# Performance work log

Hardware: AMD Instinct MI355X
Metric: run time of the kernel (lower is better)

Reference implementation:

```python
import jax, jax.numpy as jnp
import numpy as np

N_HEAD, D_K, D_V = 8, 64, 64
TOPK = 16
B, N_R, N_W = 256, 64, 64
D_READ = D_WRITE = D_OUT = 512
TEMP = float(np.power(D_K, 0.5))
EPS = 1e-7  # 10e-8 in original Sparse_attention


def sparse_attention(a, top_k):
    # a: (rows, n); RIMs Sparse_attention: threshold at k-th largest, clamp, renormalize
    if a.shape[-1] <= top_k:
        return a
    delta = jax.lax.top_k(a, top_k)[0][..., -1:] + EPS
    w = jnp.clip(a - delta, 0.0, None)
    return w / (jnp.sum(w, axis=-1, keepdims=True) + EPS)


def setup_inputs() -> dict:
    key = jax.random.key(0)
    ks = jax.random.split(key, 8)
    q = jax.random.normal(ks[0], (B, N_R, D_READ), dtype=jnp.float32)
    k = jax.random.normal(ks[1], (B, N_W, D_WRITE), dtype=jnp.float32)
    v = jax.random.normal(ks[2], (B, N_W, D_WRITE), dtype=jnp.float32)
    # GroupLinearLayer weights: (num_blocks, d_in, n_head*d)
    Wq = 0.02 * jax.random.normal(ks[3], (N_R, D_READ, N_HEAD * D_K), dtype=jnp.float32)
    Wk = 0.02 * jax.random.normal(ks[4], (N_W, D_WRITE, N_HEAD * D_K), dtype=jnp.float32)
    Wv = 0.02 * jax.random.normal(ks[5], (N_W, D_WRITE, N_HEAD * D_V), dtype=jnp.float32)
    fc_w = 0.02 * jax.random.normal(ks[6], (D_OUT, N_HEAD * D_V), dtype=jnp.float32)
    fc_b = jnp.zeros((D_OUT,), dtype=jnp.float32)
    gate_w = 0.02 * jax.random.normal(ks[7], (D_OUT, N_HEAD * D_V), dtype=jnp.float32)
    gate_b = jnp.zeros((D_OUT,), dtype=jnp.float32)
    return {"q": q, "k": k, "v": v, "Wq": Wq, "Wk": Wk, "Wv": Wv,
            "fc_w": fc_w, "fc_b": fc_b, "gate_w": gate_w, "gate_b": gate_b}


def reference(q, k, v, Wq, Wk, Wv, fc_w, fc_b, gate_w, gate_b):
    # grouped per-block projections: out[b,n] = x[b,n] @ W[n]
    qp = jnp.einsum('bnd,nde->bne', q, Wq).reshape(B, N_R, N_HEAD, D_K)
    kp = jnp.einsum('bnd,nde->bne', k, Wk).reshape(B, N_W, N_HEAD, D_K)
    vp = jnp.einsum('bnd,nde->bne', v, Wv).reshape(B, N_W, N_HEAD, D_V)
    # (H*B, len, d) with head-major leading dim, matching permute(2,0,1,3).view(-1,...)
    qh = qp.transpose(2, 0, 1, 3).reshape(N_HEAD * B, N_R, D_K)
    kh = kp.transpose(2, 0, 1, 3).reshape(N_HEAD * B, N_W, D_K)
    vh = vp.transpose(2, 0, 1, 3).reshape(N_HEAD * B, N_W, D_V)
    scores = jnp.einsum('ijk,ilk->ijl', qh, kh) / TEMP          # (HB, Nr, Nw)
    a = jnp.exp(jnp.max(scores, axis=-1, keepdims=True))        # (HB, Nr, 1)
    # flag=True: softmax over the query-block dim (permute/softmax/reshape)
    a = jax.nn.softmax(a[..., 0], axis=-1)                      # (HB, Nr)
    a = sparse_attention(a, TOPK)                               # (HB, Nr)
    attn = a[..., None]                                         # (HB, Nr, 1)
    # einsum 'ijk,ikl->ijl' with attn's k-dim == 1 broadcasts: attn * sum_k v
    out = attn * jnp.sum(vh, axis=1, keepdims=True)             # (HB, Nr, Dv)
    out = out.reshape(N_HEAD, B, N_R, D_V).transpose(1, 2, 0, 3).reshape(B, N_R, N_HEAD * D_V)
    fc_out = out @ fc_w.T + fc_b
    gate = jax.nn.sigmoid(out @ gate_w.T + gate_b)
    output = gate * jnp.tanh(fc_out)                            # residual=True gating
    return output
```

## Files before the change

### kernel.cpp

```cpp
#include <hip/hip_runtime.h>
#include <stdint.h>

#define B_    256
#define NR    64
#define NW    64
#define DIN   512
#define NH    8
#define DK    64
#define E_    512
#define TEMP_INV 0.125f
#define EPSV  1e-7f

typedef unsigned short u16;
typedef unsigned int   u32;
typedef __attribute__((ext_vector_type(4))) float  floatx4;
typedef __attribute__((ext_vector_type(8))) short  shortx8;
typedef __attribute__((ext_vector_type(4))) short  shortx4;
typedef __attribute__((ext_vector_type(2))) u32    uintx2;

__device__ __forceinline__ u32 asu(float f) { union { float f; u32 u; } c; c.f = f; return c.u; }
__device__ __forceinline__ float asf(u32 u) { union { u32 u; float f; } c; c.u = u; return c.f; }

__device__ __forceinline__ u32 packhi(u32 x, u32 y) {
    return (x >> 16) | (y & 0xFFFF0000u);
}

#define PST 40

__global__ __launch_bounds__(256)
void proj_kernel(const float* __restrict__ q, const float* __restrict__ kk_,
                 const float* __restrict__ v,
                 const float* __restrict__ Wq, const float* __restrict__ Wk,
                 const float* __restrict__ Wv,
                 float* __restrict__ qp, float* __restrict__ kp,
                 float* __restrict__ vsum)
{
    const float* X; const float* W; float* dst = nullptr; bool vmode = false;
    if (blockIdx.z == 0)      { X = q;   W = Wq; dst = qp; }
    else if (blockIdx.z == 1) { X = kk_; W = Wk; dst = kp; }
    else                      { X = v;   W = Wv; vmode = true; }

    const int n  = blockIdx.y;
    const int m0 = (blockIdx.x >> 2) * 128;
    const int n0 = (blockIdx.x & 3) * 128;

    __shared__ u16 Ah[128 * PST];
    __shared__ u16 Al[128 * PST];
    __shared__ u16 Bh[128 * PST];
    __shared__ u16 Bl[128 * PST];

    const int tid  = threadIdx.x;
    const int lane = tid & 63;
    const int wave = tid >> 6;
    const int wm   = (wave >> 1) * 64;
    const int wn   = (wave & 1) * 64;
    const int l15  = lane & 15;
    const int quad = lane >> 4;

    floatx4 acc[4][4];
#pragma unroll
    for (int i = 0; i < 4; i++)
#pragma unroll
        for (int j = 0; j < 4; j++) acc[i][j] = (floatx4){0.f, 0.f, 0.f, 0.f};

    const int arow  = tid >> 1;
    const int ahalf = tid & 1;
    const float* aptr = X + ((size_t)(m0 + arow) * NW + n) * DIN + ahalf * 16;
    const int ec0  = (tid & 31) * 4;
    const int kgrp = tid >> 5;
    const float* wbase = W + (size_t)n * (DIN * E_) + n0 + ec0;

    floatx4 pa[4], pb[4];
#pragma unroll
    for (int c = 0; c < 4; c++) pa[c] = *(const floatx4*)(aptr + c * 4);
#pragma unroll
    for (int j = 0; j < 4; j++) pb[j] = *(const floatx4*)(wbase + (size_t)(kgrp * 4 + j) * E_);

    for (int it = 0; it < 16; it++) {
        const int k0 = it * 32;

#pragma unroll
        for (int c = 0; c < 4; c++) {
            u32 x = asu(pa[c].x), y = asu(pa[c].y), z = asu(pa[c].z), w = asu(pa[c].w);
            u32 h01 = packhi(x, y), h23 = packhi(z, w);
            float r0 = pa[c].x - asf(x & 0xFFFF0000u);
            float r1 = pa[c].y - asf(y & 0xFFFF0000u);
            float r2 = pa[c].z - asf(z & 0xFFFF0000u);
            float r3 = pa[c].w - asf(w & 0xFFFF0000u);
            u32 l01 = packhi(asu(r0), asu(r1)), l23 = packhi(asu(r2), asu(r3));
            *(uintx2*)&Ah[arow * PST + ahalf * 16 + c * 4] = (uintx2){h01, h23};
            if (!vmode)
                *(uintx2*)&Al[arow * PST + ahalf * 16 + c * 4] = (uintx2){l01, l23};
        }
#pragma unroll
        for (int e = 0; e < 4; e++) {
            u32 x0 = asu(pb[0][e]), x1 = asu(pb[1][e]), x2 = asu(pb[2][e]), x3 = asu(pb[3][e]);
            u32 h01 = packhi(x0, x1), h23 = packhi(x2, x3);
            *(uintx2*)&Bh[(ec0 + e) * PST + kgrp * 4] = (uintx2){h01, h23};
            if (!vmode) {
                float r0 = pb[0][e] - asf(x0 & 0xFFFF0000u);
                float r1 = pb[1][e] - asf(x1 & 0xFFFF0000u);
                float r2 = pb[2][e] - asf(x2 & 0xFFFF0000u);
                float r3 = pb[3][e] - asf(x3 & 0xFFFF0000u);
                u32 l01 = packhi(asu(r0), asu(r1)), l23 = packhi(asu(r2), asu(r3));
                *(uintx2*)&Bl[(ec0 + e) * PST + kgrp * 4] = (uintx2){l01, l23};
            }
        }

        if (it < 15) {
            const int kn = k0 + 32;
#pragma unroll
            for (int c = 0; c < 4; c++) pa[c] = *(const floatx4*)(aptr + kn + c * 4);
#pragma unroll
            for (int j = 0; j < 4; j++)
                pb[j] = *(const floatx4*)(wbase + (size_t)(kn + kgrp * 4 + j) * E_);
        }

        __syncthreads();

        shortx8 afh[4], afl[4], bfh[4], bfl[4];
#pragma unroll
        for (int mi = 0; mi < 4; mi++) {
            afh[mi] = *(const shortx8*)&Ah[(wm + mi * 16 + l15) * PST + quad * 8];
            if (!vmode)
                afl[mi] = *(const shortx8*)&Al[(wm + mi * 16 + l15) * PST + quad * 8];
        }
#pragma unroll
        for (int ni = 0; ni < 4; ni++) {
            bfh[ni] = *(const shortx8*)&Bh[(wn + ni * 16 + l15) * PST + quad * 8];
            if (!vmode)
                bfl[ni] = *(const shortx8*)&Bl[(wn + ni * 16 + l15) * PST + quad * 8];
        }
#pragma unroll
        for (int mi = 0; mi < 4; mi++)
#pragma unroll
            for (int ni = 0; ni < 4; ni++) {
                acc[mi][ni] = __builtin_amdgcn_mfma_f32_16x16x32_bf16(
                    afh[mi], bfh[ni], acc[mi][ni], 0, 0, 0);
                if (!vmode) {
                    acc[mi][ni] = __builtin_amdgcn_mfma_f32_16x16x32_bf16(
                        afh[mi], bfl[ni], acc[mi][ni], 0, 0, 0);
                    acc[mi][ni] = __builtin_amdgcn_mfma_f32_16x16x32_bf16(
                        afl[mi], bfh[ni], acc[mi][ni], 0, 0, 0);
                }
            }
        __syncthreads();
    }

    if (!vmode) {
#pragma unroll
        for (int mi = 0; mi < 4; mi++) {
            int rowb = m0 + wm + mi * 16 + quad * 4;
#pragma unroll
            for (int ni = 0; ni < 4; ni++) {
                int col = n0 + wn + ni * 16 + l15;
#pragma unroll
                for (int r = 0; r < 4; r++)
                    dst[((size_t)(rowb + r) * NW + n) * E_ + col] = acc[mi][ni][r];
            }
        }
    } else {
#pragma unroll
        for (int mi = 0; mi < 4; mi++) {
            int rowb = m0 + wm + mi * 16 + quad * 4;
#pragma unroll
            for (int ni = 0; ni < 4; ni++) {
                int col = n0 + wn + ni * 16 + l15;
#pragma unroll
                for (int r = 0; r < 4; r++)
                    atomicAdd(&vsum[(size_t)(rowb + r) * E_ + col], acc[mi][ni][r]);
            }
        }
    }
}

__global__ __launch_bounds__(256)
void attn_kernel(const float* __restrict__ qp, const float* __restrict__ kp,
                 float* __restrict__ attnT)
{
    const int h = blockIdx.x >> 8;
    const int b = blockIdx.x & 255;

    __shared__ float qs[64 * 68];
    __shared__ float ks[64 * 68];
    __shared__ float mred[4][64];

    const int t    = threadIdx.x;
    const int w    = t >> 6;
    const int lane = t & 63;

#pragma unroll
    for (int s = 0; s < 4; s++) {
        int f = s * 256 + t;
        int row = f >> 4, c4 = (f & 15) * 4;
        *(floatx4*)&qs[row * 68 + c4] =
            *(const floatx4*)&qp[((size_t)(b * NR + row)) * E_ + h * DK + c4];
        *(floatx4*)&ks[row * 68 + c4] =
            *(const floatx4*)&kp[((size_t)(b * NW + row)) * E_ + h * DK + c4];
    }
    __syncthreads();

    floatx4 qr[16];
#pragma unroll
    for (int c = 0; c < 16; c++) qr[c] = *(const floatx4*)&qs[lane * 68 + c * 4];

    float mloc = -1e30f;
#pragma unroll 4
    for (int ll = 0; ll < 16; ll++) {
        int l = w * 16 + ll;
        floatx4 a4 = (floatx4){0.f, 0.f, 0.f, 0.f};
#pragma unroll
        for (int c = 0; c < 16; c++) {
            floatx4 kv = *(const floatx4*)&ks[l * 68 + c * 4];
            a4.x = fmaf(qr[c].x, kv.x, a4.x);
            a4.y = fmaf(qr[c].y, kv.y, a4.y);
            a4.z = fmaf(qr[c].z, kv.z, a4.z);
            a4.w = fmaf(qr[c].w, kv.w, a4.w);
        }
        float s = (a4.x + a4.y) + (a4.z + a4.w);
        mloc = fmaxf(mloc, s);
    }
    mred[w][lane] = mloc;
    __syncthreads();

    if (t < 64) {
        float m = fmaxf(fmaxf(mred[0][lane], mred[1][lane]),
                        fmaxf(mred[2][lane], mred[3][lane])) * TEMP_INV;
        float e = expf(m);
        float mx = e;
#pragma unroll
        for (int d = 1; d < 64; d <<= 1) mx = fmaxf(mx, __shfl_xor(mx, d));
        float tt = expf(e - mx);
        float S = tt;
#pragma unroll
        for (int d = 1; d < 64; d <<= 1) S += __shfl_xor(S, d);
        float s = tt / S;

        float cur = s, v16 = 0.f;
        for (int itk = 0; itk < 16; itk++) {
            float mv = cur;
#pragma unroll
            for (int d = 1; d < 64; d <<= 1) mv = fmaxf(mv, __shfl_xor(mv, d));
            unsigned long long bal = __ballot(cur == mv);
            int first = __ffsll(bal) - 1;
            if (lane == first) cur = -1e30f;
            v16 = mv;
        }
        float delta = v16 + EPSV;
        float ww = fmaxf(s - delta, 0.f);
        float sw = ww;
#pragma unroll
        for (int d = 1; d < 64; d <<= 1) sw += __shfl_xor(sw, d);
        attnT[((size_t)b * NR + lane) * NH + h] = ww / (sw + EPSV);
    }
}

__global__ __launch_bounds__(256)
void fcv_kernel(const float* __restrict__ vsum, const float* __restrict__ fc_w,
                const float* __restrict__ gate_w, float* __restrict__ fcv,
                float* __restrict__ gatev)
{
    const int ohalf = blockIdx.x >> 2;
    const int bq    = blockIdx.x & 3;
    const int h     = blockIdx.y;
    const float* W  = blockIdx.z ? gate_w : fc_w;
    float* out      = blockIdx.z ? gatev : fcv;
    const int o     = ohalf * 256 + threadIdx.x;

    __shared__ float vs[64 * 64];
#pragma unroll
    for (int i = 0; i < 16; i++) {
        int idx = i * 256 + threadIdx.x;
        int bb = idx >> 6, d = idx & 63;
        vs[idx] = vsum[(size_t)(bq * 64 + bb) * E_ + h * DK + d];
    }
    floatx4 wr[16];
#pragma unroll
    for (int c = 0; c < 16; c++)
        wr[c] = *(const floatx4*)(W + (size_t)o * E_ + h * DK + c * 4);
    __syncthreads();

    for (int bb = 0; bb < 64; bb++) {
        const floatx4* vr = (const floatx4*)&vs[bb * 64];
        float a = 0.f;
#pragma unroll
        for (int c = 0; c < 16; c++) {
            floatx4 vv = vr[c];
            a += vv.x * wr[c].x + vv.y * wr[c].y + vv.z * wr[c].z + vv.w * wr[c].w;
        }
        out[((size_t)(bq * 64 + bb) * NH + h) * E_ + o] = a;
    }
}

__global__ __launch_bounds__(256)
void final_kernel(const float* __restrict__ fcv, const float* __restrict__ gatev,
                  const float* __restrict__ attnT, const float* __restrict__ fc_b,
                  const float* __restrict__ gate_b, float* __restrict__ out)
{
    const int b = blockIdx.x;
    const int tid = threadIdx.x;
    __shared__ float ats[NR * NH];

    ats[tid]       = attnT[(size_t)b * NR * NH + tid];
    ats[256 + tid] = attnT[(size_t)b * NR * NH + 256 + tid];

    float fr[2][8], gr[2][8];
#pragma unroll
    for (int half = 0; half < 2; half++) {
        int o = half * 256 + tid;
#pragma unroll
        for (int hh = 0; hh < 8; hh++) {
            fr[half][hh] = fcv[((size_t)b * NH + hh) * E_ + o];
            gr[half][hh] = gatev[((size_t)b * NH + hh) * E_ + o];
        }
    }
    float bfc0 = fc_b[tid],   bfc1 = fc_b[256 + tid];
    float bgt0 = gate_b[tid], bgt1 = gate_b[256 + tid];
    __syncthreads();

    for (int r = 0; r < NR; r++) {
        float a[8];
#pragma unroll
        for (int hh = 0; hh < 8; hh++) a[hh] = ats[r * NH + hh];
#pragma unroll
        for (int half = 0; half < 2; half++) {
            int o = half * 256 + tid;
            float fc = half ? bfc1 : bfc0;
            float gt = half ? bgt1 : bgt0;
#pragma unroll
            for (int hh = 0; hh < 8; hh++) {
                fc = fmaf(a[hh], fr[half][hh], fc);
                gt = fmaf(a[hh], gr[half][hh], gt);
            }
            float g = 1.f / (1.f + __expf(-gt));
            out[((size_t)(b * NR + r)) * E_ + o] = g * tanhf(fc);
        }
    }
}

extern "C" void kernel_launch(void* const* d_in, const int* in_sizes, int n_in,
                              void* d_out, int out_size, void* d_ws, size_t ws_size,
                              hipStream_t stream)
{
    const float* q      = (const float*)d_in[0];
    const float* k      = (const float*)d_in[1];
    const float* v      = (const float*)d_in[2];
    const float* Wq     = (const float*)d_in[3];
    const float* Wk     = (const float*)d_in[4];
    const float* Wv     = (const float*)d_in[5];
    const float* fc_w   = (const float*)d_in[6];
    const float* fc_b   = (const float*)d_in[7];
    const float* gate_w = (const float*)d_in[8];
    const float* gate_b = (const float*)d_in[9];
    float* out = (float*)d_out;

    char* ws = (char*)d_ws;
    float* qp    = (float*)(ws);
    float* kp    = (float*)(ws + 33554432);
    float* vsum  = (float*)(ws + 67108864);
    float* attnT = (float*)(ws + 67108864 + 524288);
    float* fcv   = (float*)(ws + 67108864 + 2 * 524288);
    float* gatev = (float*)(ws + 67108864 + 2 * 524288 + 4194304);

    hipMemsetAsync(vsum, 0, 524288, stream);

    hipLaunchKernelGGL(proj_kernel, dim3(8, 64, 3), dim3(256), 0, stream,
                       q, k, v, Wq, Wk, Wv, qp, kp, vsum);
    hipLaunchKernelGGL(attn_kernel, dim3(2048), dim3(256), 0, stream, qp, kp, attnT);
    hipLaunchKernelGGL(fcv_kernel, dim3(8, 8, 2), dim3(256), 0, stream,
                       vsum, fc_w, gate_w, fcv, gatev);
    hipLaunchKernelGGL(final_kernel, dim3(256), dim3(256), 0, stream,
                       fcv, gatev, attnT, fc_b, gate_b, out);
}
```

Measured before the change: 426.2 us.

## Store q/k projections in fp16, use fdot2 attention, relayout shared tiles

The projection kernel now writes the q and k projections as fp16 instead of fp32, halving that intermediate traffic. The attention kernel reads q into registers and computes scores with packed fp16 dot products straight from global k, dropping the shared-memory staging. The projection's shared-memory tiles are relaid out in a k-chunk-major format, and its block-index mapping is reordered to group work on the same weight block. The fcv kernel gets twice as many blocks and tanh is replaced by an exp-based formula. The fp16 scores reduce precision, which risks changing the max and top-k selection.

```diff
diff --git a/kernel.cpp b/kernel.cpp
--- a/kernel.cpp
+++ b/kernel.cpp
@@ -13,41 +13,51 @@
 
 typedef unsigned short u16;
 typedef unsigned int   u32;
-typedef __attribute__((ext_vector_type(4))) float  floatx4;
-typedef __attribute__((ext_vector_type(8))) short  shortx8;
-typedef __attribute__((ext_vector_type(4))) short  shortx4;
-typedef __attribute__((ext_vector_type(2))) u32    uintx2;
+typedef _Float16 f16;
+typedef __attribute__((ext_vector_type(2))) float    floatx2;
+typedef __attribute__((ext_vector_type(4))) float    floatx4;
+typedef __attribute__((ext_vector_type(8))) short    shortx8;
+typedef __attribute__((ext_vector_type(4))) u32      uintx4;
+typedef __attribute__((ext_vector_type(2))) _Float16 halfx2;
 
 __device__ __forceinline__ u32 asu(float f) { union { float f; u32 u; } c; c.f = f; return c.u; }
 __device__ __forceinline__ float asf(u32 u) { union { u32 u; float f; } c; c.u = u; return c.f; }
-
-__device__ __forceinline__ u32 packhi(u32 x, u32 y) {
-    return (x >> 16) | (y & 0xFFFF0000u);
-}
-
-#define PST 40
+__device__ __forceinline__ u32 packhi(float x, float y) {
+    return (asu(x) >> 16) | (asu(y) & 0xFFFF0000u);
+}
+__device__ __forceinline__ float hi_of(float x) { return asf(asu(x) & 0xFFFF0000u); }
+__device__ __forceinline__ halfx2 h2(u32 u) { union { u32 u; halfx2 h; } c; c.u = u; return c.h; }
+
+#if __has_builtin(__builtin_amdgcn_fdot2)
+#define FDOT2(a, b, c) __builtin_amdgcn_fdot2((a), (b), (c), false)
+#else
+__device__ __forceinline__ float FDOT2(halfx2 a, halfx2 b, float c) {
+    return fmaf((float)a.y, (float)b.y, fmaf((float)a.x, (float)b.x, c));
+}
+#endif
 
 __global__ __launch_bounds__(256)
 void proj_kernel(const float* __restrict__ q, const float* __restrict__ kk_,
                  const float* __restrict__ v,
                  const float* __restrict__ Wq, const float* __restrict__ Wk,
                  const float* __restrict__ Wv,
-                 float* __restrict__ qp, float* __restrict__ kp,
+                 f16* __restrict__ qp, f16* __restrict__ kp,
                  float* __restrict__ vsum)
 {
-    const float* X; const float* W; float* dst = nullptr; bool vmode = false;
+    const float* X; const float* W; f16* dst = nullptr; bool vmode = false;
     if (blockIdx.z == 0)      { X = q;   W = Wq; dst = qp; }
     else if (blockIdx.z == 1) { X = kk_; W = Wk; dst = kp; }
     else                      { X = v;   W = Wv; vmode = true; }
 
-    const int n  = blockIdx.y;
-    const int m0 = (blockIdx.x >> 2) * 128;
-    const int n0 = (blockIdx.x & 3) * 128;
-
-    __shared__ u16 Ah[128 * PST];
-    __shared__ u16 Al[128 * PST];
-    __shared__ u16 Bh[128 * PST];
-    __shared__ u16 Bl[128 * PST];
+    const int n  = blockIdx.x * 8 + (blockIdx.y & 7);
+    const int t  = blockIdx.y >> 3;
+    const int m0 = (t >> 2) * 128;
+    const int n0 = (t & 3) * 128;
+
+    __shared__ u16 Ah[4096];
+    __shared__ u16 Al[4096];
+    __shared__ u16 Bh[4096];
+    __shared__ u16 Bl[4096];
 
     const int tid  = threadIdx.x;
     const int lane = tid & 63;
@@ -66,54 +76,57 @@
     const int arow  = tid >> 1;
     const int ahalf = tid & 1;
     const float* aptr = X + ((size_t)(m0 + arow) * NW + n) * DIN + ahalf * 16;
-    const int ec0  = (tid & 31) * 4;
-    const int kgrp = tid >> 5;
-    const float* wbase = W + (size_t)n * (DIN * E_) + n0 + ec0;
-
-    floatx4 pa[4], pb[4];
+    const int kq = tid >> 6;
+    const int p  = tid & 63;
+    const float* wptr = W + (size_t)n * (DIN * E_) + n0 + 2 * p;
+
+    floatx4 pa[4]; floatx2 pb[8];
 #pragma unroll
     for (int c = 0; c < 4; c++) pa[c] = *(const floatx4*)(aptr + c * 4);
 #pragma unroll
-    for (int j = 0; j < 4; j++) pb[j] = *(const floatx4*)(wbase + (size_t)(kgrp * 4 + j) * E_);
+    for (int j = 0; j < 8; j++) pb[j] = *(const floatx2*)(wptr + (size_t)(kq * 8 + j) * E_);
 
     for (int it = 0; it < 16; it++) {
-        const int k0 = it * 32;
-
-#pragma unroll
-        for (int c = 0; c < 4; c++) {
-            u32 x = asu(pa[c].x), y = asu(pa[c].y), z = asu(pa[c].z), w = asu(pa[c].w);
-            u32 h01 = packhi(x, y), h23 = packhi(z, w);
-            float r0 = pa[c].x - asf(x & 0xFFFF0000u);
-            float r1 = pa[c].y - asf(y & 0xFFFF0000u);
-            float r2 = pa[c].z - asf(z & 0xFFFF0000u);
-            float r3 = pa[c].w - asf(w & 0xFFFF0000u);
-            u32 l01 = packhi(asu(r0), asu(r1)), l23 = packhi(asu(r2), asu(r3));
-            *(uintx2*)&Ah[arow * PST + ahalf * 16 + c * 4] = (uintx2){h01, h23};
-            if (!vmode)
-                *(uintx2*)&Al[arow * PST + ahalf * 16 + c * 4] = (uintx2){l01, l23};
-        }
-#pragma unroll
-        for (int e = 0; e < 4; e++) {
-            u32 x0 = asu(pb[0][e]), x1 = asu(pb[1][e]), x2 = asu(pb[2][e]), x3 = asu(pb[3][e]);
-            u32 h01 = packhi(x0, x1), h23 = packhi(x2, x3);
-            *(uintx2*)&Bh[(ec0 + e) * PST + kgrp * 4] = (uintx2){h01, h23};
+        {
+            u32 h[8], l[8];
+#pragma unroll
+            for (int c = 0; c < 4; c++) {
+                h[2 * c]     = packhi(pa[c].x, pa[c].y);
+                h[2 * c + 1] = packhi(pa[c].z, pa[c].w);
+                float r0 = pa[c].x - hi_of(pa[c].x), r1 = pa[c].y - hi_of(pa[c].y);
+                float r2 = pa[c].z - hi_of(pa[c].z), r3 = pa[c].w - hi_of(pa[c].w);
+                l[2 * c]     = packhi(r0, r1);
+                l[2 * c + 1] = packhi(r2, r3);
+            }
+            *(uintx4*)&Ah[(2 * ahalf + 0) * 1024 + arow * 8] = (uintx4){h[0], h[1], h[2], h[3]};
+            *(uintx4*)&Ah[(2 * ahalf + 1) * 1024 + arow * 8] = (uintx4){h[4], h[5], h[6], h[7]};
             if (!vmode) {
-                float r0 = pb[0][e] - asf(x0 & 0xFFFF0000u);
-                float r1 = pb[1][e] - asf(x1 & 0xFFFF0000u);
-                float r2 = pb[2][e] - asf(x2 & 0xFFFF0000u);
-                float r3 = pb[3][e] - asf(x3 & 0xFFFF0000u);
-                u32 l01 = packhi(asu(r0), asu(r1)), l23 = packhi(asu(r2), asu(r3));
-                *(uintx2*)&Bl[(ec0 + e) * PST + kgrp * 4] = (uintx2){l01, l23};
+                *(uintx4*)&Al[(2 * ahalf + 0) * 1024 + arow * 8] = (uintx4){l[0], l[1], l[2], l[3]};
+                *(uintx4*)&Al[(2 * ahalf + 1) * 1024 + arow * 8] = (uintx4){l[4], l[5], l[6], l[7]};
+            }
+        }
+#pragma unroll
+        for (int eo = 0; eo < 2; eo++) {
+            float x0 = pb[0][eo], x1 = pb[1][eo], x2 = pb[2][eo], x3 = pb[3][eo];
+            float x4 = pb[4][eo], x5 = pb[5][eo], x6 = pb[6][eo], x7 = pb[7][eo];
+            uintx4 hv = (uintx4){packhi(x0, x1), packhi(x2, x3), packhi(x4, x5), packhi(x6, x7)};
+            *(uintx4*)&Bh[kq * 1024 + eo * 512 + p * 8] = hv;
+            if (!vmode) {
+                uintx4 lv = (uintx4){packhi(x0 - hi_of(x0), x1 - hi_of(x1)),
+                                     packhi(x2 - hi_of(x2), x3 - hi_of(x3)),
+                                     packhi(x4 - hi_of(x4), x5 - hi_of(x5)),
+                                     packhi(x6 - hi_of(x6), x7 - hi_of(x7))};
+                *(uintx4*)&Bl[kq * 1024 + eo * 512 + p * 8] = lv;
             }
         }
 
         if (it < 15) {
-            const int kn = k0 + 32;
+            const int kn = it * 32 + 32;
 #pragma unroll
             for (int c = 0; c < 4; c++) pa[c] = *(const floatx4*)(aptr + kn + c * 4);
 #pragma unroll
-            for (int j = 0; j < 4; j++)
-                pb[j] = *(const floatx4*)(wbase + (size_t)(kn + kgrp * 4 + j) * E_);
+            for (int j = 0; j < 8; j++)
+                pb[j] = *(const floatx2*)(wptr + (size_t)(kn + kq * 8 + j) * E_);
         }
 
         __syncthreads();
@@ -121,15 +134,16 @@
         shortx8 afh[4], afl[4], bfh[4], bfl[4];
 #pragma unroll
         for (int mi = 0; mi < 4; mi++) {
-            afh[mi] = *(const shortx8*)&Ah[(wm + mi * 16 + l15) * PST + quad * 8];
-            if (!vmode)
-                afl[mi] = *(const shortx8*)&Al[(wm + mi * 16 + l15) * PST + quad * 8];
+            int R = wm + mi * 16 + l15;
+            afh[mi] = *(const shortx8*)&Ah[quad * 1024 + R * 8];
+            if (!vmode) afl[mi] = *(const shortx8*)&Al[quad * 1024 + R * 8];
         }
 #pragma unroll
         for (int ni = 0; ni < 4; ni++) {
-            bfh[ni] = *(const shortx8*)&Bh[(wn + ni * 16 + l15) * PST + quad * 8];
-            if (!vmode)
-                bfl[ni] = *(const shortx8*)&Bl[(wn + ni * 16 + l15) * PST + quad * 8];
+            int e = wn + ni * 16 + l15;
+            int off = quad * 1024 + (e & 1) * 512 + (e >> 1) * 8;
+            bfh[ni] = *(const shortx8*)&Bh[off];
+            if (!vmode) bfl[ni] = *(const shortx8*)&Bl[off];
         }
 #pragma unroll
         for (int mi = 0; mi < 4; mi++)
@@ -156,7 +170,7 @@
                 int col = n0 + wn + ni * 16 + l15;
 #pragma unroll
                 for (int r = 0; r < 4; r++)
-                    dst[((size_t)(rowb + r) * NW + n) * E_ + col] = acc[mi][ni][r];
+                    dst[((size_t)(rowb + r) * NW + n) * E_ + col] = (f16)acc[mi][ni][r];
             }
         }
     } else {
@@ -175,58 +189,45 @@
 }
 
 __global__ __launch_bounds__(256)
-void attn_kernel(const float* __restrict__ qp, const float* __restrict__ kp,
+void attn_kernel(const f16* __restrict__ qp, const f16* __restrict__ kp,
                  float* __restrict__ attnT)
 {
     const int h = blockIdx.x >> 8;
     const int b = blockIdx.x & 255;
-
-    __shared__ float qs[64 * 68];
-    __shared__ float ks[64 * 68];
     __shared__ float mred[4][64];
 
     const int t    = threadIdx.x;
     const int w    = t >> 6;
     const int lane = t & 63;
 
-#pragma unroll
-    for (int s = 0; s < 4; s++) {
-        int f = s * 256 + t;
-        int row = f >> 4, c4 = (f & 15) * 4;
-        *(floatx4*)&qs[row * 68 + c4] =
-            *(const floatx4*)&qp[((size_t)(b * NR + row)) * E_ + h * DK + c4];
-        *(floatx4*)&ks[row * 68 + c4] =
-            *(const floatx4*)&kp[((size_t)(b * NW + row)) * E_ + h * DK + c4];
-    }
+    const f16* qrow = qp + ((size_t)(b * NR + lane)) * E_ + h * DK;
+    halfx2 qreg[32];
+#pragma unroll
+    for (int c = 0; c < 8; c++) {
+        uintx4 u = *(const uintx4*)(qrow + c * 8);
+        qreg[c * 4 + 0] = h2(u.x); qreg[c * 4 + 1] = h2(u.y);
+        qreg[c * 4 + 2] = h2(u.z); qreg[c * 4 + 3] = h2(u.w);
+    }
+
+    float m = -1e30f;
+    for (int ll = 0; ll < 16; ll++) {
+        int lu = __builtin_amdgcn_readfirstlane(w * 16 + ll);
+        const u32* k32 = (const u32*)(kp + ((size_t)(b * NW + lu)) * E_ + h * DK);
+        float a0 = 0.f, a1 = 0.f;
+#pragma unroll
+        for (int c = 0; c < 32; c += 2) {
+            a0 = FDOT2(qreg[c],     h2(k32[c]),     a0);
+            a1 = FDOT2(qreg[c + 1], h2(k32[c + 1]), a1);
+        }
+        m = fmaxf(m, a0 + a1);
+    }
+    mred[w][lane] = m;
     __syncthreads();
 
-    floatx4 qr[16];
-#pragma unroll
-    for (int c = 0; c < 16; c++) qr[c] = *(const floatx4*)&qs[lane * 68 + c * 4];
-
-    float mloc = -1e30f;
-#pragma unroll 4
-    for (int ll = 0; ll < 16; ll++) {
-        int l = w * 16 + ll;
-        floatx4 a4 = (floatx4){0.f, 0.f, 0.f, 0.f};
-#pragma unroll
-        for (int c = 0; c < 16; c++) {
-            floatx4 kv = *(const floatx4*)&ks[l * 68 + c * 4];
-            a4.x = fmaf(qr[c].x, kv.x, a4.x);
-            a4.y = fmaf(qr[c].y, kv.y, a4.y);
-            a4.z = fmaf(qr[c].z, kv.z, a4.z);
-            a4.w = fmaf(qr[c].w, kv.w, a4.w);
-        }
-        float s = (a4.x + a4.y) + (a4.z + a4.w);
-        mloc = fmaxf(mloc, s);
-    }
-    mred[w][lane] = mloc;
-    __syncthreads();
-
     if (t < 64) {
-        float m = fmaxf(fmaxf(mred[0][lane], mred[1][lane]),
-                        fmaxf(mred[2][lane], mred[3][lane])) * TEMP_INV;
-        float e = expf(m);
+        float mm = fmaxf(fmaxf(mred[0][lane], mred[1][lane]),
+                         fmaxf(mred[2][lane], mred[3][lane])) * TEMP_INV;
+        float e = expf(mm);
         float mx = e;
 #pragma unroll
         for (int d = 1; d < 64; d <<= 1) mx = fmaxf(mx, __shfl_xor(mx, d));
@@ -260,19 +261,19 @@
                 const float* __restrict__ gate_w, float* __restrict__ fcv,
                 float* __restrict__ gatev)
 {
-    const int ohalf = blockIdx.x >> 2;
-    const int bq    = blockIdx.x & 3;
+    const int ohalf = blockIdx.x >> 3;
+    const int bq    = blockIdx.x & 7;
     const int h     = blockIdx.y;
     const float* W  = blockIdx.z ? gate_w : fc_w;
     float* out      = blockIdx.z ? gatev : fcv;
     const int o     = ohalf * 256 + threadIdx.x;
 
-    __shared__ float vs[64 * 64];
-#pragma unroll
-    for (int i = 0; i < 16; i++) {
+    __shared__ float vs[32 * 64];
+#pragma unroll
+    for (int i = 0; i < 8; i++) {
         int idx = i * 256 + threadIdx.x;
         int bb = idx >> 6, d = idx & 63;
-        vs[idx] = vsum[(size_t)(bq * 64 + bb) * E_ + h * DK + d];
+        vs[idx] = vsum[(size_t)(bq * 32 + bb) * E_ + h * DK + d];
     }
     floatx4 wr[16];
 #pragma unroll
@@ -280,7 +281,7 @@
         wr[c] = *(const floatx4*)(W + (size_t)o * E_ + h * DK + c * 4);
     __syncthreads();
 
-    for (int bb = 0; bb < 64; bb++) {
+    for (int bb = 0; bb < 32; bb++) {
         const floatx4* vr = (const floatx4*)&vs[bb * 64];
         float a = 0.f;
 #pragma unroll
@@ -288,7 +289,7 @@
             floatx4 vv = vr[c];
             a += vv.x * wr[c].x + vv.y * wr[c].y + vv.z * wr[c].z + vv.w * wr[c].w;
         }
-        out[((size_t)(bq * 64 + bb) * NH + h) * E_ + o] = a;
+        out[((size_t)(bq * 32 + bb) * NH + h) * E_ + o] = a;
     }
 }
 
@@ -332,8 +333,10 @@
                 fc = fmaf(a[hh], fr[half][hh], fc);
                 gt = fmaf(a[hh], gr[half][hh], gt);
             }
-            float g = 1.f / (1.f + __expf(-gt));
-            out[((size_t)(b * NR + r)) * E_ + o] = g * tanhf(fc);
+            float g  = 1.f / (1.f + __expf(-gt));
+            float e2 = __expf(2.f * fc);
+            float th = 1.f - 2.f / (e2 + 1.f);
+            out[((size_t)(b * NR + r)) * E_ + o] = g * th;
         }
     }
 }
@@ -355,19 +358,19 @@
     float* out = (float*)d_out;
 
     char* ws = (char*)d_ws;
-    float* qp    = (float*)(ws);
-    float* kp    = (float*)(ws + 33554432);
-    float* vsum  = (float*)(ws + 67108864);
-    float* attnT = (float*)(ws + 67108864 + 524288);
-    float* fcv   = (float*)(ws + 67108864 + 2 * 524288);
-    float* gatev = (float*)(ws + 67108864 + 2 * 524288 + 4194304);
+    f16*   qp    = (f16*)(ws);
+    f16*   kp    = (f16*)(ws + 16777216);
+    float* vsum  = (float*)(ws + 33554432);
+    float* attnT = (float*)(ws + 33554432 + 524288);
+    float* fcv   = (float*)(ws + 33554432 + 2 * 524288);
+    float* gatev = (float*)(ws + 33554432 + 2 * 524288 + 4194304);
 
     hipMemsetAsync(vsum, 0, 524288, stream);
 
     hipLaunchKernelGGL(proj_kernel, dim3(8, 64, 3), dim3(256), 0, stream,
                        q, k, v, Wq, Wk, Wv, qp, kp, vsum);
     hipLaunchKernelGGL(attn_kernel, dim3(2048), dim3(256), 0, stream, qp, kp, attnT);
-    hipLaunchKernelGGL(fcv_kernel, dim3(8, 8, 2), dim3(256), 0, stream,
+    hipLaunchKernelGGL(fcv_kernel, dim3(16, 8, 2), dim3(256), 0, stream,
                        vsum, fc_w, gate_w, fcv, gatev);
     hipLaunchKernelGGL(final_kernel, dim3(256), dim3(256), 0, stream,
                        fcv, gatev, attnT, fc_b, gate_b, out);
```

After: 380.7 us. -10.7%, faster.
